# Kernel optimization log

Hardware: AMD Instinct MI355X
Metric: run time of the kernel (lower is better)

Reference implementation:

```python
import jax, jax.numpy as jnp
import numpy as np

S, B, L, D, H, NOP = 4, 8, 512, 128, 128, 64  # segments, batch, seg_len, input_dim, hidden, n_operators
W = S * L  # 2048 total words
FT = 0.1   # forget-gate floor


def _norm_mat(m):
    # divide each row by its count of nonzero entries (torch normalize_matrix)
    cnt = (m != 0).sum(-1, keepdims=True).astype(m.dtype)
    return m / (cnt + 1e-30)


def _l2(x):
    return x / (jnp.linalg.norm(x, axis=-1, keepdims=True) + 1e-30)


def setup_inputs() -> dict:
    key = jax.random.key(0)
    ks = jax.random.split(key, 16)
    word_outputs = jax.random.normal(ks[0], (S, B, L, D), jnp.float32)
    node_hidden = jax.random.normal(ks[1], (B, D), jnp.float32)
    op_embedding = jax.random.normal(ks[2], (B, NOP, D), jnp.float32)
    word_operator = (jax.random.uniform(ks[3], (B, W, NOP)) < 0.05).astype(jnp.float32)
    word_word = (jax.random.uniform(ks[4], (B, W, W)) < 0.02).astype(jnp.float32)
    depend_relation = (jax.random.uniform(ks[5], (S, B, L, L)) < 0.05).astype(jnp.float32)
    word_exist_matrix = (jax.random.uniform(ks[6], (B, W, W)) < 0.9).astype(jnp.float32)
    word_exist_sequence = (jax.random.uniform(ks[7], (B, W)) < 0.9).astype(jnp.float32)
    goal_word = (jax.random.uniform(ks[8], (B, W)) < 0.2).astype(jnp.float32)

    def lin(k, fi, fo):
        k1, k2 = jax.random.split(k)
        s = 1.0 / np.sqrt(fi).astype(np.float32)
        return (jax.random.uniform(k1, (fi, fo), jnp.float32, -s, s),
                jax.random.uniform(k2, (fo,), jnp.float32, -s, s))

    o_w_W, o_w_b = lin(ks[9], D, H)
    wk_W, wk_b = lin(ks[10], D, H)
    ws_W, ws_b = lin(ks[11], D, H)
    up_W, up_b = lin(ks[12], 3 * H, D)
    wg_W, wg_b = lin(ks[13], D, D)
    fg_W, fg_b = lin(ks[14], 2 * D, D)
    return dict(word_outputs=word_outputs, node_hidden=node_hidden, op_embedding=op_embedding,
                word_operator=word_operator, word_word=word_word, depend_relation=depend_relation,
                word_exist_matrix=word_exist_matrix, word_exist_sequence=word_exist_sequence,
                goal_word=goal_word, o_w_W=o_w_W, o_w_b=o_w_b, wk_W=wk_W, wk_b=wk_b,
                ws_W=ws_W, ws_b=ws_b, up_W=up_W, up_b=up_b, wg_W=wg_W, wg_b=wg_b,
                fg_W=fg_W, fg_b=fg_b)


def reference(word_outputs, node_hidden, op_embedding, word_operator, word_word,
              depend_relation, word_exist_matrix, word_exist_sequence, goal_word,
              o_w_W, o_w_b, wk_W, wk_b, ws_W, ws_b, up_W, up_b, wg_W, wg_b, fg_W, fg_b):
    # cat(word_outputs, dim=1) -> [B, W, D]
    all_word = word_outputs.transpose(1, 0, 2, 3).reshape(B, W, D)
    # operator aggregation: [B,W,NOP] @ o_w(op_embedding) -> [B,W,H], L2-normalized
    word_o = _l2(jnp.einsum('bwo,boh->bwh', word_operator, op_embedding @ o_w_W + o_w_b))
    # knowledge aggregation over masked word-word adjacency
    adj_k = _norm_mat(word_word * word_exist_matrix)
    word_w_k = _l2(jnp.einsum('bvw,bwh->bvh', adj_k, all_word @ wk_W + wk_b))
    # per-segment dependency aggregation, then concat along word dim
    seg = jnp.einsum('sbij,sbjh->sbih', _norm_mat(depend_relation), word_outputs @ ws_W + ws_b)
    word_w_s = _l2(seg.transpose(1, 0, 2, 3).reshape(B, W, H))
    neighbor = jnp.concatenate([word_o, word_w_k, word_w_s], axis=-1)  # [B, W, 3H]
    word_updated = jax.nn.relu(neighbor @ up_W + up_b)  # [B, W, D]
    # goal pooling: bmm([B,1,W],[B,W,D]) -> [B,D]
    gw = _norm_mat(goal_word * word_exist_sequence)
    goal_w = jnp.einsum('bw,bwd->bd', gw, word_updated)
    goal_updated = jax.nn.relu(goal_w @ wg_W + wg_b)
    forget = jax.nn.sigmoid(jnp.concatenate([goal_w, node_hidden], axis=-1) @ fg_W + fg_b)
    return jnp.maximum(forget, FT) * node_hidden + (1.0 - forget) * goal_updated
```

## Files before the change

kernel.cpp:

```cpp
#include <hip/hip_runtime.h>
#include <math.h>

#define Sn 4
#define Bn 8
#define Ln 512
#define Dn 128
#define Hn 128
#define NOPn 64
#define Wn 2048


__device__ __forceinline__ float bf2f(unsigned short u) {
    return __uint_as_float(((unsigned int)u) << 16);
}
__device__ __forceinline__ unsigned short f2bf(float f) {
    unsigned int u = __float_as_uint(f);
    return (unsigned short)((u + 0x7FFFu + ((u >> 16) & 1u)) >> 16);
}

__global__ __launch_bounds__(256) void gemm_small(const float* __restrict__ A,
                                                  const float* __restrict__ Wm,
                                                  const float* __restrict__ bias,
                                                  unsigned short* __restrict__ C) {
    __shared__ __align__(16) float lA[32][68];
    __shared__ __align__(16) float lW[32][132];
    const int tid = threadIdx.x;
    const int m0 = blockIdx.x * 64;
    float acc[4][8] = {};
    const int r0 = (tid & 15) * 4;
    const int h0 = (tid >> 4) * 8;
    for (int k0 = 0; k0 < 128; k0 += 32) {
        __syncthreads();
        {
            const int r = tid >> 2, kk = (tid & 3) * 8;
            const float* src = A + (size_t)(m0 + r) * 128 + (k0 + kk);
            float4 v0 = reinterpret_cast<const float4*>(src)[0];
            float4 v1 = reinterpret_cast<const float4*>(src)[1];
            lA[kk + 0][r] = v0.x; lA[kk + 1][r] = v0.y;
            lA[kk + 2][r] = v0.z; lA[kk + 3][r] = v0.w;
            lA[kk + 4][r] = v1.x; lA[kk + 5][r] = v1.y;
            lA[kk + 6][r] = v1.z; lA[kk + 7][r] = v1.w;
        }
        {
            const int kk = tid >> 3, hh = (tid & 7) * 16;
            const float* src = Wm + (size_t)(k0 + kk) * 128 + hh;
#pragma unroll
            for (int q = 0; q < 4; ++q) {
                float4 v = reinterpret_cast<const float4*>(src)[q];
                lW[kk][hh + 4 * q + 0] = v.x; lW[kk][hh + 4 * q + 1] = v.y;
                lW[kk][hh + 4 * q + 2] = v.z; lW[kk][hh + 4 * q + 3] = v.w;
            }
        }
        __syncthreads();
#pragma unroll
        for (int k = 0; k < 32; ++k) {
            float4 a  = *reinterpret_cast<const float4*>(&lA[k][r0]);
            float4 w0 = *reinterpret_cast<const float4*>(&lW[k][h0]);
            float4 w1 = *reinterpret_cast<const float4*>(&lW[k][h0 + 4]);
            float av[4] = {a.x, a.y, a.z, a.w};
            float wv[8] = {w0.x, w0.y, w0.z, w0.w, w1.x, w1.y, w1.z, w1.w};
#pragma unroll
            for (int i = 0; i < 4; ++i)
#pragma unroll
                for (int j = 0; j < 8; ++j) acc[i][j] = fmaf(av[i], wv[j], acc[i][j]);
        }
    }
#pragma unroll
    for (int i = 0; i < 4; ++i) {
        alignas(16) unsigned short us[8];
#pragma unroll
        for (int j = 0; j < 8; ++j) us[j] = f2bf(acc[i][j] + bias[h0 + j]);
        *reinterpret_cast<uint4*>(C + (size_t)(m0 + r0 + i) * 128 + h0) =
            *reinterpret_cast<const uint4*>(us);
    }
}

__global__ __launch_bounds__(256) void gemm2_k(const float* __restrict__ A,
                                               const float* __restrict__ W1,
                                               const float* __restrict__ W2,
                                               const float* __restrict__ b1,
                                               const float* __restrict__ b2,
                                               unsigned short* __restrict__ C1,
                                               unsigned short* __restrict__ C2) {
    __shared__ __align__(16) float lA[32][68];
    __shared__ __align__(16) float lW1[32][132];
    __shared__ __align__(16) float lW2[32][132];
    const int tid = threadIdx.x;
    const int m0 = blockIdx.x * 64;
    float acc1[4][8] = {}, acc2[4][8] = {};
    const int r0 = (tid & 15) * 4;
    const int h0 = (tid >> 4) * 8;
    for (int k0 = 0; k0 < 128; k0 += 32) {
        __syncthreads();
        {
            const int r = tid >> 2, kk = (tid & 3) * 8;
            const float* src = A + (size_t)(m0 + r) * 128 + (k0 + kk);
            float4 v0 = reinterpret_cast<const float4*>(src)[0];
            float4 v1 = reinterpret_cast<const float4*>(src)[1];
            lA[kk + 0][r] = v0.x; lA[kk + 1][r] = v0.y;
            lA[kk + 2][r] = v0.z; lA[kk + 3][r] = v0.w;
            lA[kk + 4][r] = v1.x; lA[kk + 5][r] = v1.y;
            lA[kk + 6][r] = v1.z; lA[kk + 7][r] = v1.w;
        }
        {
            const int kk = tid >> 3, hh = (tid & 7) * 16;
            const float* s1 = W1 + (size_t)(k0 + kk) * 128 + hh;
            const float* s2 = W2 + (size_t)(k0 + kk) * 128 + hh;
#pragma unroll
            for (int q = 0; q < 4; ++q) {
                float4 v1 = reinterpret_cast<const float4*>(s1)[q];
                float4 v2 = reinterpret_cast<const float4*>(s2)[q];
                lW1[kk][hh + 4 * q + 0] = v1.x; lW1[kk][hh + 4 * q + 1] = v1.y;
                lW1[kk][hh + 4 * q + 2] = v1.z; lW1[kk][hh + 4 * q + 3] = v1.w;
                lW2[kk][hh + 4 * q + 0] = v2.x; lW2[kk][hh + 4 * q + 1] = v2.y;
                lW2[kk][hh + 4 * q + 2] = v2.z; lW2[kk][hh + 4 * q + 3] = v2.w;
            }
        }
        __syncthreads();
#pragma unroll
        for (int k = 0; k < 32; ++k) {
            float4 a   = *reinterpret_cast<const float4*>(&lA[k][r0]);
            float4 w10 = *reinterpret_cast<const float4*>(&lW1[k][h0]);
            float4 w11 = *reinterpret_cast<const float4*>(&lW1[k][h0 + 4]);
            float4 w20 = *reinterpret_cast<const float4*>(&lW2[k][h0]);
            float4 w21 = *reinterpret_cast<const float4*>(&lW2[k][h0 + 4]);
            float av[4] = {a.x, a.y, a.z, a.w};
            float wv1[8] = {w10.x, w10.y, w10.z, w10.w, w11.x, w11.y, w11.z, w11.w};
            float wv2[8] = {w20.x, w20.y, w20.z, w20.w, w21.x, w21.y, w21.z, w21.w};
#pragma unroll
            for (int i = 0; i < 4; ++i)
#pragma unroll
                for (int j = 0; j < 8; ++j) {
                    acc1[i][j] = fmaf(av[i], wv1[j], acc1[i][j]);
                    acc2[i][j] = fmaf(av[i], wv2[j], acc2[i][j]);
                }
        }
    }
#pragma unroll
    for (int i = 0; i < 4; ++i) {
        alignas(16) unsigned short u1[8], u2[8];
#pragma unroll
        for (int j = 0; j < 8; ++j) {
            u1[j] = f2bf(acc1[i][j] + b1[h0 + j]);
            u2[j] = f2bf(acc2[i][j] + b2[h0 + j]);
        }
        const size_t off = (size_t)(m0 + r0 + i) * 128 + h0;
        *reinterpret_cast<uint4*>(C1 + off) = *reinterpret_cast<const uint4*>(u1);
        *reinterpret_cast<uint4*>(C2 + off) = *reinterpret_cast<const uint4*>(u2);
    }
}

__global__ __launch_bounds__(256) void compact_k(const float* __restrict__ goal,
                                                 const float* __restrict__ wes,
                                                 int* __restrict__ widx,
                                                 int* __restrict__ wcnt) {
    const int b = blockIdx.x, t = threadIdx.x;
    __shared__ int cnt;
    if (t == 0) cnt = 0;
    __syncthreads();
#pragma unroll
    for (int j = 0; j < 8; ++j) {
        const int w = t * 8 + j;
        if (goal[b * Wn + w] != 0.f && wes[b * Wn + w] != 0.f) {
            const int p = atomicAdd(&cnt, 1);
            if (p < 1024) widx[b * 1024 + p] = w;
        }
    }
    __syncthreads();
    if (t == 0) wcnt[b] = cnt < 1024 ? cnt : 1024;
}

__global__ __launch_bounds__(256) void mega_agg(const int* __restrict__ widx,
                                                const int* __restrict__ wcnt,
                                                const float* __restrict__ ww,
                                                const float* __restrict__ wem,
                                                const float* __restrict__ dep,
                                                const float* __restrict__ wop,
                                                const unsigned short* __restrict__ oph,
                                                const unsigned short* __restrict__ wkh,
                                                const unsigned short* __restrict__ wsh,
                                                unsigned short* __restrict__ nbc) {
    const int slot = blockIdx.x;
    const int b = slot >> 10, i = slot & 1023;
    if (i >= wcnt[b]) return;
    const int w_dst = widx[slot];
    const int t = threadIdx.x;
    const int lane = t & 63, wv = t >> 6;

    __shared__ int kidx[512];
    __shared__ int keep[512];
    __shared__ int sidx[256];
    __shared__ int kn, sn;
    __shared__ float part1[4][128];
    __shared__ float part2[4][128];
    if (t == 0) { kn = 0; sn = 0; }
    __syncthreads();

    const float* wwr = ww + ((size_t)(b * Wn + w_dst)) * Wn;
#pragma unroll
    for (int q = 0; q < 2; ++q) {
        const int e0 = q * 1024 + t * 4;
        float4 v = *reinterpret_cast<const float4*>(wwr + e0);
        float vv[4] = {v.x, v.y, v.z, v.w};
#pragma unroll
        for (int j = 0; j < 4; ++j)
            if (vv[j] != 0.f) {
                int p = atomicAdd(&kn, 1);
                if (p < 512) kidx[p] = e0 + j;
            }
    }
    const int sD = w_dst >> 9, lD = w_dst & 511;
    if (t < 128) {
        const float* dr = dep + ((size_t)((sD * Bn + b) * Ln + lD)) * Ln + t * 4;
        float4 v = *reinterpret_cast<const float4*>(dr);
        float vv[4] = {v.x, v.y, v.z, v.w};
#pragma unroll
        for (int j = 0; j < 4; ++j)
            if (vv[j] != 0.f) {
                int p = atomicAdd(&sn, 1);
                if (p < 256) sidx[p] = t * 4 + j;
            }
    }
    float m_op = 0.f;
    if (wv == 3) m_op = wop[((size_t)(b * Wn + w_dst)) * NOPn + lane];
    __syncthreads();

    const int nk = kn < 512 ? kn : 512;
    const int ns = sn < 256 ? sn : 256;
    for (int p = t; p < nk; p += 256)
        keep[p] = (wem[((size_t)(b * Wn + w_dst)) * Wn + kidx[p]] != 0.f) ? 1 : 0;
    __syncthreads();

    {
        float a0 = 0.f, a1 = 0.f;
        for (int p = wv; p < nk; p += 4)
            if (keep[p]) {
                const int w = kidx[p];
                const int s = w >> 9, l = w & 511;
                ushort2 x = *reinterpret_cast<const ushort2*>(
                    wkh + ((size_t)((s * Bn + b) * Ln + l)) * Hn + 2 * lane);
                a0 += bf2f(x.x);
                a1 += bf2f(x.y);
            }
        part1[wv][2 * lane]     = a0;
        part1[wv][2 * lane + 1] = a1;
    }
    {
        const unsigned short* base = wsh + (size_t)((sD * Bn + b) * Ln) * Hn + 2 * lane;
        float a0 = 0.f, a1 = 0.f;
        for (int p = wv; p < ns; p += 4) {
            ushort2 x = *reinterpret_cast<const ushort2*>(base + (size_t)sidx[p] * Hn);
            a0 += bf2f(x.x);
            a1 += bf2f(x.y);
        }
        part2[wv][2 * lane]     = a0;
        part2[wv][2 * lane + 1] = a1;
    }
    if (wv == 3) {
        unsigned long long bal = __ballot(m_op != 0.f);
        float a0 = 0.f, a1 = 0.f;
        const unsigned short* base = oph + (size_t)b * NOPn * Hn + 2 * lane;
        while (bal) {
            const int o = __ffsll(bal) - 1;
            bal &= bal - 1;
            ushort2 v = *reinterpret_cast<const ushort2*>(base + o * Hn);
            a0 += bf2f(v.x);
            a1 += bf2f(v.y);
        }
        float ss = a0 * a0 + a1 * a1;
#pragma unroll
        for (int off = 1; off < 64; off <<= 1) ss += __shfl_xor(ss, off);
        const float sc = 1.f / (sqrtf(ss) + 1e-30f);
        ushort2 o2 = {f2bf(a0 * sc), f2bf(a1 * sc)};
        *reinterpret_cast<ushort2*>(nbc + (size_t)slot * 384 + 2 * lane) = o2;
    }
    __syncthreads();

    if (wv == 0) {
        float s0 = 0.f, s1 = 0.f;
#pragma unroll
        for (int q = 0; q < 4; ++q) {
            s0 += part1[q][2 * lane];
            s1 += part1[q][2 * lane + 1];
        }
        float ss = s0 * s0 + s1 * s1;
#pragma unroll
        for (int off = 1; off < 64; off <<= 1) ss += __shfl_xor(ss, off);
        const float sc = 1.f / (sqrtf(ss) + 1e-30f);
        ushort2 o2 = {f2bf(s0 * sc), f2bf(s1 * sc)};
        *reinterpret_cast<ushort2*>(nbc + (size_t)slot * 384 + 128 + 2 * lane) = o2;
    } else if (wv == 1) {
        float s0 = 0.f, s1 = 0.f;
#pragma unroll
        for (int q = 0; q < 4; ++q) {
            s0 += part2[q][2 * lane];
            s1 += part2[q][2 * lane + 1];
        }
        float ss = s0 * s0 + s1 * s1;
#pragma unroll
        for (int off = 1; off < 64; off <<= 1) ss += __shfl_xor(ss, off);
        const float sc = 1.f / (sqrtf(ss) + 1e-30f);
        ushort2 o2 = {f2bf(s0 * sc), f2bf(s1 * sc)};
        *reinterpret_cast<ushort2*>(nbc + (size_t)slot * 384 + 256 + 2 * lane) = o2;
    }
}

__global__ __launch_bounds__(256) void up_gemm_c(const unsigned short* __restrict__ A,
                                                 const float* __restrict__ Wm,
                                                 const float* __restrict__ bias,
                                                 const int* __restrict__ wcnt,
                                                 float* __restrict__ C) {
    const int m0 = blockIdx.x * 64;
    if ((m0 & 1023) >= wcnt[m0 >> 10]) return;
    __shared__ __align__(16) float lA[32][68];
    __shared__ __align__(16) float lW[32][132];
    const int tid = threadIdx.x;
    float acc[4][8] = {};
    const int r0 = (tid & 15) * 4;
    const int h0 = (tid >> 4) * 8;
    for (int k0 = 0; k0 < 384; k0 += 32) {
        __syncthreads();
        {
            const int r = tid >> 2, kk = (tid & 3) * 8;
            const unsigned short* src = A + (size_t)(m0 + r) * 384 + (k0 + kk);
            alignas(16) unsigned short us[8];
            *reinterpret_cast<uint4*>(us) = *reinterpret_cast<const uint4*>(src);
#pragma unroll
            for (int j = 0; j < 8; ++j) lA[kk + j][r] = bf2f(us[j]);
        }
        {
            const int kk = tid >> 3, hh = (tid & 7) * 16;
            const float* src = Wm + (size_t)(k0 + kk) * 128 + hh;
#pragma unroll
            for (int q = 0; q < 4; ++q) {
                float4 v = reinterpret_cast<const float4*>(src)[q];
                lW[kk][hh + 4 * q + 0] = v.x; lW[kk][hh + 4 * q + 1] = v.y;
                lW[kk][hh + 4 * q + 2] = v.z; lW[kk][hh + 4 * q + 3] = v.w;
            }
        }
        __syncthreads();
#pragma unroll
        for (int k = 0; k < 32; ++k) {
            float4 a  = *reinterpret_cast<const float4*>(&lA[k][r0]);
            float4 w0 = *reinterpret_cast<const float4*>(&lW[k][h0]);
            float4 w1 = *reinterpret_cast<const float4*>(&lW[k][h0 + 4]);
            float av[4] = {a.x, a.y, a.z, a.w};
            float wv[8] = {w0.x, w0.y, w0.z, w0.w, w1.x, w1.y, w1.z, w1.w};
#pragma unroll
            for (int i = 0; i < 4; ++i)
#pragma unroll
                for (int j = 0; j < 8; ++j) acc[i][j] = fmaf(av[i], wv[j], acc[i][j]);
        }
    }
#pragma unroll
    for (int i = 0; i < 4; ++i) {
        float o[8];
#pragma unroll
        for (int j = 0; j < 8; ++j) o[j] = fmaxf(acc[i][j] + bias[h0 + j], 0.f);
        float* dst = C + (size_t)(m0 + r0 + i) * 128 + h0;
        *reinterpret_cast<float4*>(dst)     = reinterpret_cast<float4&>(o[0]);
        *reinterpret_cast<float4*>(dst + 4) = reinterpret_cast<float4&>(o[4]);
    }
}

__global__ __launch_bounds__(1024) void final3_k(const int* __restrict__ wcnt,
                                                 const float* __restrict__ wuc,
                                                 const float* __restrict__ nh,
                                                 const float* __restrict__ wgW,
                                                 const float* __restrict__ wgb,
                                                 const float* __restrict__ fgW,
                                                 const float* __restrict__ fgb,
                                                 float* __restrict__ out) {
    const int b = blockIdx.x, t = threadIdx.x;
    const int d = t & 127, sl = t >> 7;
    __shared__ float red[1024];
    __shared__ float gw[Dn], nhs[Dn];
    const int n = wcnt[b];
    float acc = 0.f;
    for (int p = sl; p < n; p += 8) acc += wuc[((size_t)(b * 1024 + p)) * Dn + d];
    red[t] = acc;
    __syncthreads();
    for (int s = 512; s >= 128; s >>= 1) {
        if (t < s) red[t] += red[t + s];
        __syncthreads();
    }
    if (t < 128) {
        gw[t] = red[t] / ((float)n + 1e-30f);
        nhs[t] = nh[b * Dn + t];
    }
    __syncthreads();
    float pg = 0.f;
    for (int k = sl * 16; k < sl * 16 + 16; ++k) pg = fmaf(gw[k], wgW[k * Dn + d], pg);
    red[t] = pg;
    __syncthreads();
    for (int s = 512; s >= 128; s >>= 1) {
        if (t < s) red[t] += red[t + s];
        __syncthreads();
    }
    float gu = 0.f;
    if (t < 128) gu = fmaxf(red[t] + wgb[t], 0.f);
    __syncthreads();
    float pf = 0.f;
    for (int kk = sl * 32; kk < sl * 32 + 32; ++kk) {
        const float x = (kk < 128) ? gw[kk] : nhs[kk - 128];
        pf = fmaf(x, fgW[(size_t)kk * Dn + d], pf);
    }
    red[t] = pf;
    __syncthreads();
    for (int s = 512; s >= 128; s >>= 1) {
        if (t < s) red[t] += red[t + s];
        __syncthreads();
    }
    if (t < 128) {
        const float fg = red[t] + fgb[t];
        const float forget = 1.f / (1.f + expf(-fg));
        out[b * Dn + t] = fmaxf(forget, 0.1f) * nhs[t] + (1.f - forget) * gu;
    }
}

extern "C" void kernel_launch(void* const* d_in, const int* in_sizes, int n_in,
                              void* d_out, int out_size, void* d_ws, size_t ws_size,
                              hipStream_t stream) {
    (void)in_sizes; (void)n_in; (void)out_size; (void)ws_size;
    const float* word_outputs        = (const float*)d_in[0];
    const float* node_hidden         = (const float*)d_in[1];
    const float* op_embedding        = (const float*)d_in[2];
    const float* word_operator       = (const float*)d_in[3];
    const float* word_word           = (const float*)d_in[4];
    const float* depend_relation     = (const float*)d_in[5];
    const float* word_exist_matrix   = (const float*)d_in[6];
    const float* word_exist_sequence = (const float*)d_in[7];
    const float* goal_word           = (const float*)d_in[8];
    const float* o_w_W = (const float*)d_in[9];
    const float* o_w_b = (const float*)d_in[10];
    const float* wk_W  = (const float*)d_in[11];
    const float* wk_b  = (const float*)d_in[12];
    const float* ws_W  = (const float*)d_in[13];
    const float* ws_b  = (const float*)d_in[14];
    const float* up_W  = (const float*)d_in[15];
    const float* up_b  = (const float*)d_in[16];
    const float* wg_W  = (const float*)d_in[17];
    const float* wg_b  = (const float*)d_in[18];
    const float* fg_W  = (const float*)d_in[19];
    const float* fg_b  = (const float*)d_in[20];
    float* out = (float*)d_out;

    char* ws = (char*)d_ws;
    unsigned short* oph = (unsigned short*)(ws + 0);
    unsigned short* wkh = (unsigned short*)(ws + (1u << 20));
    unsigned short* wsh = (unsigned short*)(ws + (5u << 20));
    int* widx           = (int*)(ws + (9u << 20));
    int* wcnt           = (int*)(ws + (9u << 20) + 32768);
    unsigned short* nbc = (unsigned short*)(ws + (10u << 20));
    float* wuc          = (float*)(ws + (17u << 20));

    gemm_small<<<8, 256, 0, stream>>>(op_embedding, o_w_W, o_w_b, oph);
    gemm2_k<<<256, 256, 0, stream>>>(word_outputs, wk_W, ws_W, wk_b, ws_b, wkh, wsh);
    compact_k<<<8, 256, 0, stream>>>(goal_word, word_exist_sequence, widx, wcnt);
    mega_agg<<<8192, 256, 0, stream>>>(widx, wcnt, word_word, word_exist_matrix,
                                       depend_relation, word_operator, oph, wkh, wsh, nbc);
    up_gemm_c<<<128, 256, 0, stream>>>(nbc, up_W, up_b, wcnt, wuc);
    final3_k<<<8, 1024, 0, stream>>>(wcnt, wuc, node_hidden,
                                     wg_W, wg_b, fg_W, fg_b, out);
}
```

Before: 381.0 us.

## Merge prep kernels and fuse up-projection with goal pooling and final gating

Folds the two projection GEMMs and the goal-word compaction into one launch that dispatches on block index, and also zeroes a new accumulator there. The up-projection kernel now pools its ReLU output per column into a global accumulator with atomics, instead of writing the full result to memory for a separate pass. The last block to finish, found with a done counter, runs the small goal and forget-gate matmuls. This cuts the launch count from six to three and drops the intermediate buffer, at the cost of float atomics that make the pooled sums order-dependent and a serial tail run by a single block.

```diff
diff --git a/kernel.cpp b/kernel.cpp
--- a/kernel.cpp
+++ b/kernel.cpp
@@ -18,156 +18,159 @@
     return (unsigned short)((u + 0x7FFFu + ((u >> 16) & 1u)) >> 16);
 }
 
-__global__ __launch_bounds__(256) void gemm_small(const float* __restrict__ A,
-                                                  const float* __restrict__ Wm,
-                                                  const float* __restrict__ bias,
-                                                  unsigned short* __restrict__ C) {
-    __shared__ __align__(16) float lA[32][68];
-    __shared__ __align__(16) float lW[32][132];
-    const int tid = threadIdx.x;
-    const int m0 = blockIdx.x * 64;
-    float acc[4][8] = {};
-    const int r0 = (tid & 15) * 4;
-    const int h0 = (tid >> 4) * 8;
-    for (int k0 = 0; k0 < 128; k0 += 32) {
-        __syncthreads();
-        {
-            const int r = tid >> 2, kk = (tid & 3) * 8;
-            const float* src = A + (size_t)(m0 + r) * 128 + (k0 + kk);
-            float4 v0 = reinterpret_cast<const float4*>(src)[0];
-            float4 v1 = reinterpret_cast<const float4*>(src)[1];
-            lA[kk + 0][r] = v0.x; lA[kk + 1][r] = v0.y;
-            lA[kk + 2][r] = v0.z; lA[kk + 3][r] = v0.w;
-            lA[kk + 4][r] = v1.x; lA[kk + 5][r] = v1.y;
-            lA[kk + 6][r] = v1.z; lA[kk + 7][r] = v1.w;
-        }
-        {
-            const int kk = tid >> 3, hh = (tid & 7) * 16;
-            const float* src = Wm + (size_t)(k0 + kk) * 128 + hh;
-#pragma unroll
-            for (int q = 0; q < 4; ++q) {
-                float4 v = reinterpret_cast<const float4*>(src)[q];
-                lW[kk][hh + 4 * q + 0] = v.x; lW[kk][hh + 4 * q + 1] = v.y;
-                lW[kk][hh + 4 * q + 2] = v.z; lW[kk][hh + 4 * q + 3] = v.w;
-            }
-        }
-        __syncthreads();
-#pragma unroll
-        for (int k = 0; k < 32; ++k) {
-            float4 a  = *reinterpret_cast<const float4*>(&lA[k][r0]);
-            float4 w0 = *reinterpret_cast<const float4*>(&lW[k][h0]);
-            float4 w1 = *reinterpret_cast<const float4*>(&lW[k][h0 + 4]);
-            float av[4] = {a.x, a.y, a.z, a.w};
-            float wv[8] = {w0.x, w0.y, w0.z, w0.w, w1.x, w1.y, w1.z, w1.w};
-#pragma unroll
-            for (int i = 0; i < 4; ++i)
-#pragma unroll
-                for (int j = 0; j < 8; ++j) acc[i][j] = fmaf(av[i], wv[j], acc[i][j]);
-        }
-    }
-#pragma unroll
-    for (int i = 0; i < 4; ++i) {
-        alignas(16) unsigned short us[8];
-#pragma unroll
-        for (int j = 0; j < 8; ++j) us[j] = f2bf(acc[i][j] + bias[h0 + j]);
-        *reinterpret_cast<uint4*>(C + (size_t)(m0 + r0 + i) * 128 + h0) =
-            *reinterpret_cast<const uint4*>(us);
-    }
-}
-
-__global__ __launch_bounds__(256) void gemm2_k(const float* __restrict__ A,
-                                               const float* __restrict__ W1,
-                                               const float* __restrict__ W2,
-                                               const float* __restrict__ b1,
-                                               const float* __restrict__ b2,
-                                               unsigned short* __restrict__ C1,
-                                               unsigned short* __restrict__ C2) {
+__global__ __launch_bounds__(256) void prep_k(const float* __restrict__ A,
+                                              const float* __restrict__ W1,
+                                              const float* __restrict__ W2,
+                                              const float* __restrict__ b1,
+                                              const float* __restrict__ b2,
+                                              unsigned short* __restrict__ C1,
+                                              unsigned short* __restrict__ C2,
+                                              const float* __restrict__ ope,
+                                              const float* __restrict__ owW,
+                                              const float* __restrict__ owb,
+                                              unsigned short* __restrict__ oph,
+                                              const float* __restrict__ goal,
+                                              const float* __restrict__ wes,
+                                              int* __restrict__ widx,
+                                              int* __restrict__ wcnt,
+                                              float* __restrict__ gwacc,
+                                              int* __restrict__ done) {
     __shared__ __align__(16) float lA[32][68];
     __shared__ __align__(16) float lW1[32][132];
     __shared__ __align__(16) float lW2[32][132];
-    const int tid = threadIdx.x;
-    const int m0 = blockIdx.x * 64;
-    float acc1[4][8] = {}, acc2[4][8] = {};
-    const int r0 = (tid & 15) * 4;
-    const int h0 = (tid >> 4) * 8;
-    for (int k0 = 0; k0 < 128; k0 += 32) {
+    __shared__ int cnt;
+    const int bid = blockIdx.x, tid = threadIdx.x;
+
+    if (bid < 256) {
+        const int m0 = bid * 64;
+        float acc1[4][8] = {}, acc2[4][8] = {};
+        const int r0 = (tid & 15) * 4;
+        const int h0 = (tid >> 4) * 8;
+        for (int k0 = 0; k0 < 128; k0 += 32) {
+            __syncthreads();
+            {
+                const int r = tid >> 2, kk = (tid & 3) * 8;
+                const float* src = A + (size_t)(m0 + r) * 128 + (k0 + kk);
+                float4 v0 = reinterpret_cast<const float4*>(src)[0];
+                float4 v1 = reinterpret_cast<const float4*>(src)[1];
+                lA[kk + 0][r] = v0.x; lA[kk + 1][r] = v0.y;
+                lA[kk + 2][r] = v0.z; lA[kk + 3][r] = v0.w;
+                lA[kk + 4][r] = v1.x; lA[kk + 5][r] = v1.y;
+                lA[kk + 6][r] = v1.z; lA[kk + 7][r] = v1.w;
+            }
+            {
+                const int kk = tid >> 3, hh = (tid & 7) * 16;
+                const float* s1 = W1 + (size_t)(k0 + kk) * 128 + hh;
+                const float* s2 = W2 + (size_t)(k0 + kk) * 128 + hh;
+#pragma unroll
+                for (int q = 0; q < 4; ++q) {
+                    float4 v1 = reinterpret_cast<const float4*>(s1)[q];
+                    float4 v2 = reinterpret_cast<const float4*>(s2)[q];
+                    lW1[kk][hh + 4 * q + 0] = v1.x; lW1[kk][hh + 4 * q + 1] = v1.y;
+                    lW1[kk][hh + 4 * q + 2] = v1.z; lW1[kk][hh + 4 * q + 3] = v1.w;
+                    lW2[kk][hh + 4 * q + 0] = v2.x; lW2[kk][hh + 4 * q + 1] = v2.y;
+                    lW2[kk][hh + 4 * q + 2] = v2.z; lW2[kk][hh + 4 * q + 3] = v2.w;
+                }
+            }
+            __syncthreads();
+#pragma unroll
+            for (int k = 0; k < 32; ++k) {
+                float4 a   = *reinterpret_cast<const float4*>(&lA[k][r0]);
+                float4 w10 = *reinterpret_cast<const float4*>(&lW1[k][h0]);
+                float4 w11 = *reinterpret_cast<const float4*>(&lW1[k][h0 + 4]);
+                float4 w20 = *reinterpret_cast<const float4*>(&lW2[k][h0]);
+                float4 w21 = *reinterpret_cast<const float4*>(&lW2[k][h0 + 4]);
+                float av[4] = {a.x, a.y, a.z, a.w};
+                float wv1[8] = {w10.x, w10.y, w10.z, w10.w, w11.x, w11.y, w11.z, w11.w};
+                float wv2[8] = {w20.x, w20.y, w20.z, w20.w, w21.x, w21.y, w21.z, w21.w};
+#pragma unroll
+                for (int i = 0; i < 4; ++i)
+#pragma unroll
+                    for (int j = 0; j < 8; ++j) {
+                        acc1[i][j] = fmaf(av[i], wv1[j], acc1[i][j]);
+                        acc2[i][j] = fmaf(av[i], wv2[j], acc2[i][j]);
+                    }
+            }
+        }
+#pragma unroll
+        for (int i = 0; i < 4; ++i) {
+            alignas(16) unsigned short u1[8], u2[8];
+#pragma unroll
+            for (int j = 0; j < 8; ++j) {
+                u1[j] = f2bf(acc1[i][j] + b1[h0 + j]);
+                u2[j] = f2bf(acc2[i][j] + b2[h0 + j]);
+            }
+            const size_t off = (size_t)(m0 + r0 + i) * 128 + h0;
+            *reinterpret_cast<uint4*>(C1 + off) = *reinterpret_cast<const uint4*>(u1);
+            *reinterpret_cast<uint4*>(C2 + off) = *reinterpret_cast<const uint4*>(u2);
+        }
+    } else if (bid < 264) {
+        const int m0 = (bid - 256) * 64;
+        float acc[4][8] = {};
+        const int r0 = (tid & 15) * 4;
+        const int h0 = (tid >> 4) * 8;
+        for (int k0 = 0; k0 < 128; k0 += 32) {
+            __syncthreads();
+            {
+                const int r = tid >> 2, kk = (tid & 3) * 8;
+                const float* src = ope + (size_t)(m0 + r) * 128 + (k0 + kk);
+                float4 v0 = reinterpret_cast<const float4*>(src)[0];
+                float4 v1 = reinterpret_cast<const float4*>(src)[1];
+                lA[kk + 0][r] = v0.x; lA[kk + 1][r] = v0.y;
+                lA[kk + 2][r] = v0.z; lA[kk + 3][r] = v0.w;
+                lA[kk + 4][r] = v1.x; lA[kk + 5][r] = v1.y;
+                lA[kk + 6][r] = v1.z; lA[kk + 7][r] = v1.w;
+            }
+            {
+                const int kk = tid >> 3, hh = (tid & 7) * 16;
+                const float* src = owW + (size_t)(k0 + kk) * 128 + hh;
+#pragma unroll
+                for (int q = 0; q < 4; ++q) {
+                    float4 v = reinterpret_cast<const float4*>(src)[q];
+                    lW1[kk][hh + 4 * q + 0] = v.x; lW1[kk][hh + 4 * q + 1] = v.y;
+                    lW1[kk][hh + 4 * q + 2] = v.z; lW1[kk][hh + 4 * q + 3] = v.w;
+                }
+            }
+            __syncthreads();
+#pragma unroll
+            for (int k = 0; k < 32; ++k) {
+                float4 a  = *reinterpret_cast<const float4*>(&lA[k][r0]);
+                float4 w0 = *reinterpret_cast<const float4*>(&lW1[k][h0]);
+                float4 w1 = *reinterpret_cast<const float4*>(&lW1[k][h0 + 4]);
+                float av[4] = {a.x, a.y, a.z, a.w};
+                float wv[8] = {w0.x, w0.y, w0.z, w0.w, w1.x, w1.y, w1.z, w1.w};
+#pragma unroll
+                for (int i = 0; i < 4; ++i)
+#pragma unroll
+                    for (int j = 0; j < 8; ++j) acc[i][j] = fmaf(av[i], wv[j], acc[i][j]);
+            }
+        }
+#pragma unroll
+        for (int i = 0; i < 4; ++i) {
+            alignas(16) unsigned short us[8];
+#pragma unroll
+            for (int j = 0; j < 8; ++j) us[j] = f2bf(acc[i][j] + owb[h0 + j]);
+            *reinterpret_cast<uint4*>(oph + (size_t)(m0 + r0 + i) * 128 + h0) =
+                *reinterpret_cast<const uint4*>(us);
+        }
+    } else if (bid < 272) {
+        const int b = bid - 264;
+        if (tid == 0) cnt = 0;
         __syncthreads();
-        {
-            const int r = tid >> 2, kk = (tid & 3) * 8;
-            const float* src = A + (size_t)(m0 + r) * 128 + (k0 + kk);
-            float4 v0 = reinterpret_cast<const float4*>(src)[0];
-            float4 v1 = reinterpret_cast<const float4*>(src)[1];
-            lA[kk + 0][r] = v0.x; lA[kk + 1][r] = v0.y;
-            lA[kk + 2][r] = v0.z; lA[kk + 3][r] = v0.w;
-            lA[kk + 4][r] = v1.x; lA[kk + 5][r] = v1.y;
-            lA[kk + 6][r] = v1.z; lA[kk + 7][r] = v1.w;
-        }
-        {
-            const int kk = tid >> 3, hh = (tid & 7) * 16;
-            const float* s1 = W1 + (size_t)(k0 + kk) * 128 + hh;
-            const float* s2 = W2 + (size_t)(k0 + kk) * 128 + hh;
-#pragma unroll
-            for (int q = 0; q < 4; ++q) {
-                float4 v1 = reinterpret_cast<const float4*>(s1)[q];
-                float4 v2 = reinterpret_cast<const float4*>(s2)[q];
-                lW1[kk][hh + 4 * q + 0] = v1.x; lW1[kk][hh + 4 * q + 1] = v1.y;
-                lW1[kk][hh + 4 * q + 2] = v1.z; lW1[kk][hh + 4 * q + 3] = v1.w;
-                lW2[kk][hh + 4 * q + 0] = v2.x; lW2[kk][hh + 4 * q + 1] = v2.y;
-                lW2[kk][hh + 4 * q + 2] = v2.z; lW2[kk][hh + 4 * q + 3] = v2.w;
+#pragma unroll
+        for (int j = 0; j < 8; ++j) {
+            const int w = tid * 8 + j;
+            if (goal[b * Wn + w] != 0.f && wes[b * Wn + w] != 0.f) {
+                const int p = atomicAdd(&cnt, 1);
+                if (p < 1024) widx[b * 1024 + p] = w;
             }
         }
         __syncthreads();
-#pragma unroll
-        for (int k = 0; k < 32; ++k) {
-            float4 a   = *reinterpret_cast<const float4*>(&lA[k][r0]);
-            float4 w10 = *reinterpret_cast<const float4*>(&lW1[k][h0]);
-            float4 w11 = *reinterpret_cast<const float4*>(&lW1[k][h0 + 4]);
-            float4 w20 = *reinterpret_cast<const float4*>(&lW2[k][h0]);
-            float4 w21 = *reinterpret_cast<const float4*>(&lW2[k][h0 + 4]);
-            float av[4] = {a.x, a.y, a.z, a.w};
-            float wv1[8] = {w10.x, w10.y, w10.z, w10.w, w11.x, w11.y, w11.z, w11.w};
-            float wv2[8] = {w20.x, w20.y, w20.z, w20.w, w21.x, w21.y, w21.z, w21.w};
-#pragma unroll
-            for (int i = 0; i < 4; ++i)
-#pragma unroll
-                for (int j = 0; j < 8; ++j) {
-                    acc1[i][j] = fmaf(av[i], wv1[j], acc1[i][j]);
-                    acc2[i][j] = fmaf(av[i], wv2[j], acc2[i][j]);
-                }
-        }
-    }
-#pragma unroll
-    for (int i = 0; i < 4; ++i) {
-        alignas(16) unsigned short u1[8], u2[8];
-#pragma unroll
-        for (int j = 0; j < 8; ++j) {
-            u1[j] = f2bf(acc1[i][j] + b1[h0 + j]);
-            u2[j] = f2bf(acc2[i][j] + b2[h0 + j]);
-        }
-        const size_t off = (size_t)(m0 + r0 + i) * 128 + h0;
-        *reinterpret_cast<uint4*>(C1 + off) = *reinterpret_cast<const uint4*>(u1);
-        *reinterpret_cast<uint4*>(C2 + off) = *reinterpret_cast<const uint4*>(u2);
-    }
-}
-
-__global__ __launch_bounds__(256) void compact_k(const float* __restrict__ goal,
-                                                 const float* __restrict__ wes,
-                                                 int* __restrict__ widx,
-                                                 int* __restrict__ wcnt) {
-    const int b = blockIdx.x, t = threadIdx.x;
-    __shared__ int cnt;
-    if (t == 0) cnt = 0;
-    __syncthreads();
-#pragma unroll
-    for (int j = 0; j < 8; ++j) {
-        const int w = t * 8 + j;
-        if (goal[b * Wn + w] != 0.f && wes[b * Wn + w] != 0.f) {
-            const int p = atomicAdd(&cnt, 1);
-            if (p < 1024) widx[b * 1024 + p] = w;
-        }
-    }
-    __syncthreads();
-    if (t == 0) wcnt[b] = cnt < 1024 ? cnt : 1024;
+        if (tid == 0) wcnt[b] = cnt < 1024 ? cnt : 1024;
+    } else {
+        for (int idx = tid; idx < 1024; idx += 256) gwacc[idx] = 0.f;
+        if (tid == 0) *done = 0;
+    }
 }
 
 __global__ __launch_bounds__(256) void mega_agg(const int* __restrict__ widx,
@@ -305,116 +308,113 @@
     }
 }
 
-__global__ __launch_bounds__(256) void up_gemm_c(const unsigned short* __restrict__ A,
-                                                 const float* __restrict__ Wm,
-                                                 const float* __restrict__ bias,
-                                                 const int* __restrict__ wcnt,
-                                                 float* __restrict__ C) {
-    const int m0 = blockIdx.x * 64;
-    if ((m0 & 1023) >= wcnt[m0 >> 10]) return;
+__global__ __launch_bounds__(256) void up_final_k(const unsigned short* __restrict__ nbc,
+                                                  const float* __restrict__ upW,
+                                                  const float* __restrict__ upb,
+                                                  const int* __restrict__ wcnt,
+                                                  float* __restrict__ gwacc,
+                                                  int* __restrict__ done,
+                                                  const float* __restrict__ nh,
+                                                  const float* __restrict__ wgW,
+                                                  const float* __restrict__ wgb,
+                                                  const float* __restrict__ fgW,
+                                                  const float* __restrict__ fgb,
+                                                  float* __restrict__ out) {
     __shared__ __align__(16) float lA[32][68];
     __shared__ __align__(16) float lW[32][132];
-    const int tid = threadIdx.x;
-    float acc[4][8] = {};
+    __shared__ float colsum[128];
+    __shared__ float gwl[1024];
+    __shared__ float nhl[1024];
+    __shared__ int lastFlag;
+    const int bid = blockIdx.x, tid = threadIdx.x;
+    const int m0 = bid * 64;
+    const int b = m0 >> 10;
+    const int cnt = wcnt[b];
     const int r0 = (tid & 15) * 4;
     const int h0 = (tid >> 4) * 8;
-    for (int k0 = 0; k0 < 384; k0 += 32) {
+
+    if ((m0 & 1023) < cnt) {
+        float acc[4][8] = {};
+        for (int k0 = 0; k0 < 384; k0 += 32) {
+            __syncthreads();
+            {
+                const int r = tid >> 2, kk = (tid & 3) * 8;
+                const unsigned short* src = nbc + (size_t)(m0 + r) * 384 + (k0 + kk);
+                alignas(16) unsigned short us[8];
+                *reinterpret_cast<uint4*>(us) = *reinterpret_cast<const uint4*>(src);
+#pragma unroll
+                for (int j = 0; j < 8; ++j) lA[kk + j][r] = bf2f(us[j]);
+            }
+            {
+                const int kk = tid >> 3, hh = (tid & 7) * 16;
+                const float* src = upW + (size_t)(k0 + kk) * 128 + hh;
+#pragma unroll
+                for (int q = 0; q < 4; ++q) {
+                    float4 v = reinterpret_cast<const float4*>(src)[q];
+                    lW[kk][hh + 4 * q + 0] = v.x; lW[kk][hh + 4 * q + 1] = v.y;
+                    lW[kk][hh + 4 * q + 2] = v.z; lW[kk][hh + 4 * q + 3] = v.w;
+                }
+            }
+            __syncthreads();
+#pragma unroll
+            for (int k = 0; k < 32; ++k) {
+                float4 a  = *reinterpret_cast<const float4*>(&lA[k][r0]);
+                float4 w0 = *reinterpret_cast<const float4*>(&lW[k][h0]);
+                float4 w1 = *reinterpret_cast<const float4*>(&lW[k][h0 + 4]);
+                float av[4] = {a.x, a.y, a.z, a.w};
+                float wv[8] = {w0.x, w0.y, w0.z, w0.w, w1.x, w1.y, w1.z, w1.w};
+#pragma unroll
+                for (int i = 0; i < 4; ++i)
+#pragma unroll
+                    for (int j = 0; j < 8; ++j) acc[i][j] = fmaf(av[i], wv[j], acc[i][j]);
+            }
+        }
+        if (tid < 128) colsum[tid] = 0.f;
         __syncthreads();
-        {
-            const int r = tid >> 2, kk = (tid & 3) * 8;
-            const unsigned short* src = A + (size_t)(m0 + r) * 384 + (k0 + kk);
-            alignas(16) unsigned short us[8];
-            *reinterpret_cast<uint4*>(us) = *reinterpret_cast<const uint4*>(src);
-#pragma unroll
-            for (int j = 0; j < 8; ++j) lA[kk + j][r] = bf2f(us[j]);
-        }
-        {
-            const int kk = tid >> 3, hh = (tid & 7) * 16;
-            const float* src = Wm + (size_t)(k0 + kk) * 128 + hh;
-#pragma unroll
-            for (int q = 0; q < 4; ++q) {
-                float4 v = reinterpret_cast<const float4*>(src)[q];
-                lW[kk][hh + 4 * q + 0] = v.x; lW[kk][hh + 4 * q + 1] = v.y;
-                lW[kk][hh + 4 * q + 2] = v.z; lW[kk][hh + 4 * q + 3] = v.w;
-            }
-        }
+        float part[8] = {};
+#pragma unroll
+        for (int i = 0; i < 4; ++i) {
+            const int m = m0 + r0 + i;
+            if ((m & 1023) < cnt) {
+#pragma unroll
+                for (int j = 0; j < 8; ++j)
+                    part[j] += fmaxf(acc[i][j] + upb[h0 + j], 0.f);
+            }
+        }
+#pragma unroll
+        for (int j = 0; j < 8; ++j) atomicAdd(&colsum[h0 + j], part[j]);
         __syncthreads();
-#pragma unroll
-        for (int k = 0; k < 32; ++k) {
-            float4 a  = *reinterpret_cast<const float4*>(&lA[k][r0]);
-            float4 w0 = *reinterpret_cast<const float4*>(&lW[k][h0]);
-            float4 w1 = *reinterpret_cast<const float4*>(&lW[k][h0 + 4]);
-            float av[4] = {a.x, a.y, a.z, a.w};
-            float wv[8] = {w0.x, w0.y, w0.z, w0.w, w1.x, w1.y, w1.z, w1.w};
-#pragma unroll
-            for (int i = 0; i < 4; ++i)
-#pragma unroll
-                for (int j = 0; j < 8; ++j) acc[i][j] = fmaf(av[i], wv[j], acc[i][j]);
-        }
-    }
-#pragma unroll
-    for (int i = 0; i < 4; ++i) {
-        float o[8];
-#pragma unroll
-        for (int j = 0; j < 8; ++j) o[j] = fmaxf(acc[i][j] + bias[h0 + j], 0.f);
-        float* dst = C + (size_t)(m0 + r0 + i) * 128 + h0;
-        *reinterpret_cast<float4*>(dst)     = reinterpret_cast<float4&>(o[0]);
-        *reinterpret_cast<float4*>(dst + 4) = reinterpret_cast<float4&>(o[4]);
-    }
-}
-
-__global__ __launch_bounds__(1024) void final3_k(const int* __restrict__ wcnt,
-                                                 const float* __restrict__ wuc,
-                                                 const float* __restrict__ nh,
-                                                 const float* __restrict__ wgW,
-                                                 const float* __restrict__ wgb,
-                                                 const float* __restrict__ fgW,
-                                                 const float* __restrict__ fgb,
-                                                 float* __restrict__ out) {
-    const int b = blockIdx.x, t = threadIdx.x;
-    const int d = t & 127, sl = t >> 7;
-    __shared__ float red[1024];
-    __shared__ float gw[Dn], nhs[Dn];
-    const int n = wcnt[b];
-    float acc = 0.f;
-    for (int p = sl; p < n; p += 8) acc += wuc[((size_t)(b * 1024 + p)) * Dn + d];
-    red[t] = acc;
-    __syncthreads();
-    for (int s = 512; s >= 128; s >>= 1) {
-        if (t < s) red[t] += red[t + s];
-        __syncthreads();
-    }
-    if (t < 128) {
-        gw[t] = red[t] / ((float)n + 1e-30f);
-        nhs[t] = nh[b * Dn + t];
-    }
-    __syncthreads();
-    float pg = 0.f;
-    for (int k = sl * 16; k < sl * 16 + 16; ++k) pg = fmaf(gw[k], wgW[k * Dn + d], pg);
-    red[t] = pg;
-    __syncthreads();
-    for (int s = 512; s >= 128; s >>= 1) {
-        if (t < s) red[t] += red[t + s];
-        __syncthreads();
-    }
-    float gu = 0.f;
-    if (t < 128) gu = fmaxf(red[t] + wgb[t], 0.f);
-    __syncthreads();
-    float pf = 0.f;
-    for (int kk = sl * 32; kk < sl * 32 + 32; ++kk) {
-        const float x = (kk < 128) ? gw[kk] : nhs[kk - 128];
-        pf = fmaf(x, fgW[(size_t)kk * Dn + d], pf);
-    }
-    red[t] = pf;
-    __syncthreads();
-    for (int s = 512; s >= 128; s >>= 1) {
-        if (t < s) red[t] += red[t + s];
-        __syncthreads();
-    }
-    if (t < 128) {
-        const float fg = red[t] + fgb[t];
+        if (tid < 128) atomicAdd(&gwacc[b * 128 + tid], colsum[tid]);
+    }
+    __threadfence();
+    if (tid == 0) {
+        const int old = atomicAdd(done, 1);
+        lastFlag = (old == (int)gridDim.x - 1);
+    }
+    __syncthreads();
+    if (!lastFlag) return;
+    __threadfence();
+    for (int idx = tid; idx < 1024; idx += 256) {
+        const int bb = idx >> 7;
+        const float n = (float)wcnt[bb] + 1e-30f;
+        gwl[idx] = atomicAdd(&gwacc[idx], 0.f) / n;
+        nhl[idx] = nh[idx];
+    }
+    __syncthreads();
+#pragma unroll
+    for (int q = 0; q < 4; ++q) {
+        const int o = q * 256 + tid;
+        const int b2 = o >> 7, d = o & 127;
+        const float* gwp = &gwl[b2 * 128];
+        const float* nhp = &nhl[b2 * 128];
+        float gu = wgb[d];
+        for (int k = 0; k < 128; ++k) gu = fmaf(gwp[k], wgW[k * 128 + d], gu);
+        gu = fmaxf(gu, 0.f);
+        float fg = fgb[d];
+        for (int k = 0; k < 128; ++k) fg = fmaf(gwp[k], fgW[k * 128 + d], fg);
+        for (int k = 0; k < 128; ++k) fg = fmaf(nhp[k], fgW[(128 + k) * 128 + d], fg);
         const float forget = 1.f / (1.f + expf(-fg));
-        out[b * Dn + t] = fmaxf(forget, 0.1f) * nhs[t] + (1.f - forget) * gu;
+        out[o] = fmaxf(forget, 0.1f) * nhp[d] + (1.f - forget) * gu;
     }
 }
 
@@ -451,15 +451,16 @@
     unsigned short* wsh = (unsigned short*)(ws + (5u << 20));
     int* widx           = (int*)(ws + (9u << 20));
     int* wcnt           = (int*)(ws + (9u << 20) + 32768);
+    float* gwacc        = (float*)(ws + (9u << 20) + 65536);
+    int* done           = (int*)(ws + (9u << 20) + 131072);
     unsigned short* nbc = (unsigned short*)(ws + (10u << 20));
-    float* wuc          = (float*)(ws + (17u << 20));
-
-    gemm_small<<<8, 256, 0, stream>>>(op_embedding, o_w_W, o_w_b, oph);
-    gemm2_k<<<256, 256, 0, stream>>>(word_outputs, wk_W, ws_W, wk_b, ws_b, wkh, wsh);
-    compact_k<<<8, 256, 0, stream>>>(goal_word, word_exist_sequence, widx, wcnt);
+
+    prep_k<<<273, 256, 0, stream>>>(word_outputs, wk_W, ws_W, wk_b, ws_b, wkh, wsh,
+                                    op_embedding, o_w_W, o_w_b, oph,
+                                    goal_word, word_exist_sequence, widx, wcnt,
+                                    gwacc, done);
     mega_agg<<<8192, 256, 0, stream>>>(widx, wcnt, word_word, word_exist_matrix,
                                        depend_relation, word_operator, oph, wkh, wsh, nbc);
-    up_gemm_c<<<128, 256, 0, stream>>>(nbc, up_W, up_b, wcnt, wuc);
-    final3_k<<<8, 1024, 0, stream>>>(wcnt, wuc, node_hidden,
-                                     wg_W, wg_b, fg_W, fg_b, out);
-}
+    up_final_k<<<128, 256, 0, stream>>>(nbc, up_W, up_b, wcnt, gwacc, done,
+                                        node_hidden, wg_W, wg_b, fg_W, fg_b, out);
+}
```

Result: no change. 388.1 us (+1.9%).
